# Optimization experiments

Measured on AMD Instinct MI355X. Metric: run time of the kernel, lower is better.

The kernel has to match this reference:

```python
import jax, jax.numpy as jnp
import numpy as np

N, K, F_IN, F_OUT = 32768, 16, 128, 128
NEG_SLOPE = 0.2  # LeakyReLU slope in original module


def setup_inputs() -> dict:
    key = jax.random.key(0)
    ks = jax.random.split(key, 8)
    nodes = jax.random.normal(ks[0], (N, F_IN), dtype=jnp.float32)
    neighbors = jax.random.normal(ks[1], (N, K, F_IN), dtype=jnp.float32)
    aspects = jax.random.normal(ks[2], (N, K, F_IN), dtype=jnp.float32)
    attention_scores = jax.random.uniform(ks[3], (N, K), dtype=jnp.float32)
    # Parameters (torch.nn.Linear stores weight as [out, in])
    lim_w = float(np.sqrt(6.0 / (F_IN + F_OUT)))  # xavier_uniform
    W = jax.random.uniform(ks[4], (F_OUT, F_IN), minval=-lim_w, maxval=lim_w, dtype=jnp.float32)
    lim_a = float(np.sqrt(6.0 / (2 * F_IN + F_OUT)))
    Wa = jax.random.uniform(ks[5], (F_OUT, 2 * F_IN), minval=-lim_a, maxval=lim_a, dtype=jnp.float32)
    ba = jax.random.uniform(ks[6], (F_OUT,), minval=-0.05, maxval=0.05, dtype=jnp.float32)
    bias = jnp.zeros((F_OUT,), dtype=jnp.float32)
    return {"nodes": nodes, "neighbors": neighbors, "aspects": aspects,
            "attention_scores": attention_scores, "W": W, "Wa": Wa, "ba": ba, "bias": bias}


def reference(nodes, neighbors, aspects, attention_scores, W, Wa, ba, bias):
    # linear_proj (no bias); dropout(p=0.01) treated as eval/identity
    node_proj = nodes @ W.T                                  # [N, F_OUT]
    neigh_proj = jnp.einsum('nkf,of->nko', neighbors, W)     # [N, K, F_OUT]
    asp_proj = jnp.einsum('nkf,of->nko', aspects, W)         # [N, K, F_OUT]
    # aspects_method == 'linear': cat(neigh_proj, asp_proj) then Linear(2F->F)
    cat = jnp.concatenate([neigh_proj, asp_proj], axis=-1)   # [N, K, 2*F_OUT]
    nap = jnp.einsum('nkf,of->nko', cat, Wa) + ba            # [N, K, F_OUT]
    # per-edge: leakyReLU(nap + broadcast target node proj).exp()
    features_per_edge = jnp.exp(jax.nn.leaky_relu(nap + node_proj[:, None, :], NEG_SLOPE))
    # weight by attention score and sum over neighbors (scatter-sum per node)
    out = jnp.sum(features_per_edge * attention_scores[..., None], axis=1)  # [N, F_OUT]
    # skip_concat_bias: concat=True -> view [N, F_OUT], add bias, ELU activation
    return jax.nn.elu(out + bias)
```

## Files before the change

kernel.cpp:

```cpp
#include <hip/hip_runtime.h>
#include <hip/hip_bf16.h>
#include <stdint.h>

typedef short bf16x8 __attribute__((ext_vector_type(8)));
typedef float f32x4  __attribute__((ext_vector_type(4)));

#define NNODES    32768
#define KNB       16
#define FDIM      128
#define NEG_SLOPE 0.2f
#define NBLK      512
#define PPB       (NNODES / (2 * NBLK))

static __device__ __forceinline__ unsigned short f2bf(float x) {
  union { float f; unsigned u; } v; v.f = x;
  unsigned r = v.u + 0x7fffu + ((v.u >> 16) & 1u);
  return (unsigned short)(r >> 16);
}

static __device__ __forceinline__ bf16x8 pack8(f32x4 lo, f32x4 hi) {
  union { __hip_bfloat162 h[4]; bf16x8 v; } u;
  u.h[0] = __float22bfloat162_rn(make_float2(lo[0], lo[1]));
  u.h[1] = __float22bfloat162_rn(make_float2(lo[2], lo[3]));
  u.h[2] = __float22bfloat162_rn(make_float2(hi[0], hi[1]));
  u.h[3] = __float22bfloat162_rn(make_float2(hi[2], hi[3]));
  return u.v;
}

static __device__ __forceinline__ void storeBL(unsigned short* BL, int ct, int l16,
                                               int col, unsigned short v) {
  const int kc = col >> 5, quad = (col >> 3) & 3, j = col & 7;
  BL[(size_t)(((kc * 8 + ct) * 64) + quad * 16 + l16) * 8 + j] = v;
}

__global__ void prep_weights(const float* __restrict__ W,
                             const float* __restrict__ Wa,
                             unsigned short* __restrict__ BL) {
  const int o = blockIdx.x;
  const int f = threadIdx.x;
  const float* war = Wa + o * 256;
  float a1 = 0.f, a2 = 0.f;
  #pragma unroll 8
  for (int j = 0; j < 128; ++j) {
    float w = W[j * 128 + f];
    a1 = fmaf(war[j], w, a1);
    a2 = fmaf(war[128 + j], w, a2);
  }
  const int ct = o >> 4, l16 = o & 15;
  storeBL(BL, ct, l16, f,       f2bf(a1));
  storeBL(BL, ct, l16, 128 + f, f2bf(a2));
  storeBL(BL, ct, l16, 256 + f, f2bf(W[o * 128 + f]));
}

__global__ __launch_bounds__(512, 4)
void grn_main(const float* __restrict__ nodes,
              const float* __restrict__ neighbors,
              const float* __restrict__ aspects,
              const float* __restrict__ scores,
              const unsigned short* __restrict__ BL,
              const float* __restrict__ ba,
              const float* __restrict__ bias,
              float* __restrict__ out) {
  const int tid  = threadIdx.x;
  const int lane = tid & 63;
  const int w    = tid >> 6;
  const int quad = lane >> 4;
  const int l16  = lane & 15;

  __shared__ __align__(16) unsigned short Aeg[2][8192];
  __shared__ __align__(16) unsigned short And[2][256];
  __shared__ float xp[2][2][FDIM];

  bf16x8 breg[12];
  #pragma unroll
  for (int kc = 0; kc < 12; ++kc)
    breg[kc] = *(const bf16x8*)(BL + ((size_t)(kc * 8 + w) * 64 + lane) * 8);

  const float ba_c = ba[w * 16 + l16];
  float bias_t = 0.f;
  if (tid < 256) bias_t = bias[tid & 127];

  const int seg = tid >> 8;
  const int row = (tid >> 4) & 15;
  const int c16 = tid & 15;
  const int cc  = seg * 16 + c16;
  const float* segp = seg ? aspects : neighbors;
  const int wroff = row * 512 + ((cc * 16) ^ ((row & 7) << 4));
  const int sw    = (l16 & 7) << 4;
  const int rdrow = l16 * 512;

  const int pair0 = blockIdx.x * PPB;

  f32x4 eg[2][2];
  f32x4 nd[2];

  {
    const size_t ng = (size_t)pair0 * 2;
    #pragma unroll
    for (int n = 0; n < 2; ++n) {
      const float* src = segp + ((ng + n) * KNB + row) * FDIM + c16 * 8;
      eg[n][0] = *(const f32x4*)src;
      eg[n][1] = *(const f32x4*)(src + 4);
    }
    if (tid < 32) {
      const float* nsrc = nodes + (ng + (tid >> 4)) * FDIM + (tid & 15) * 8;
      nd[0] = *(const f32x4*)nsrc;
      nd[1] = *(const f32x4*)(nsrc + 4);
    }
    #pragma unroll
    for (int n = 0; n < 2; ++n)
      *(bf16x8*)((char*)Aeg[0] + n * 8192 + wroff) = pack8(eg[n][0], eg[n][1]);
    if (tid < 32)
      *(bf16x8*)((char*)And[0] + tid * 16) = pack8(nd[0], nd[1]);
  }
  __syncthreads();

  for (int i = 0; i < PPB; ++i) {
    const int buf = i & 1;
    const size_t ng = (size_t)(pair0 + i) * 2;

    if (i + 1 < PPB) {
      const size_t ng2 = ng + 2;
      #pragma unroll
      for (int n = 0; n < 2; ++n) {
        const float* src = segp + ((ng2 + n) * KNB + row) * FDIM + c16 * 8;
        eg[n][0] = *(const f32x4*)src;
        eg[n][1] = *(const f32x4*)(src + 4);
      }
      if (tid < 32) {
        const float* nsrc = nodes + (ng2 + (tid >> 4)) * FDIM + (tid & 15) * 8;
        nd[0] = *(const f32x4*)nsrc;
        nd[1] = *(const f32x4*)(nsrc + 4);
      }
    }

    f32x4 acc[2];
    acc[0] = (f32x4){0.f, 0.f, 0.f, 0.f};
    acc[1] = (f32x4){0.f, 0.f, 0.f, 0.f};
    const char* ab = (const char*)Aeg[buf];
    const char* nb = (const char*)And[buf];
    #pragma unroll
    for (int n = 0; n < 2; ++n) {
      #pragma unroll
      for (int kc = 0; kc < 8; ++kc) {
        bf16x8 af = *(const bf16x8*)(ab + n * 8192 + rdrow +
                                     (((kc * 4 + quad) * 16) ^ sw));
        acc[n] = __builtin_amdgcn_mfma_f32_16x16x32_bf16(af, breg[kc], acc[n], 0, 0, 0);
      }
      #pragma unroll
      for (int kn = 0; kn < 4; ++kn) {
        bf16x8 af = *(const bf16x8*)(nb + (n * 16 + kn * 4 + quad) * 16);
        acc[n] = __builtin_amdgcn_mfma_f32_16x16x32_bf16(af, breg[8 + kn], acc[n], 0, 0, 0);
      }
    }

    #pragma unroll
    for (int n = 0; n < 2; ++n) {
      f32x4 sc = *(const f32x4*)(scores + (ng + n) * KNB + quad * 4);
      float s = 0.f;
      #pragma unroll
      for (int r = 0; r < 4; ++r) {
        float t  = acc[n][r] + ba_c;
        float lr = t > 0.f ? t : NEG_SLOPE * t;
        s = fmaf(__expf(lr), sc[r], s);
      }
      s += __shfl_xor(s, 16);
      s += __shfl_xor(s, 32);
      if (quad == 0) xp[buf][n][w * 16 + l16] = s;
    }

    if (i + 1 < PPB) {
      const int nbuf = buf ^ 1;
      #pragma unroll
      for (int n = 0; n < 2; ++n)
        *(bf16x8*)((char*)Aeg[nbuf] + n * 8192 + wroff) = pack8(eg[n][0], eg[n][1]);
      if (tid < 32)
        *(bf16x8*)((char*)And[nbuf] + tid * 16) = pack8(nd[0], nd[1]);
    }
    __syncthreads();

    if (tid < 256) {
      const int n = tid >> 7, c = tid & 127;
      float v = xp[buf][n][c] + bias_t;
      v = v > 0.f ? v : __expf(v) - 1.f;
      out[(ng + n) * FDIM + c] = v;
    }
  }
}

extern "C" void kernel_launch(void* const* d_in, const int* in_sizes, int n_in,
                              void* d_out, int out_size, void* d_ws, size_t ws_size,
                              hipStream_t stream) {
  const float* nodes     = (const float*)d_in[0];
  const float* neighbors = (const float*)d_in[1];
  const float* aspects   = (const float*)d_in[2];
  const float* scores    = (const float*)d_in[3];
  const float* W         = (const float*)d_in[4];
  const float* Wa        = (const float*)d_in[5];
  const float* ba        = (const float*)d_in[6];
  const float* bias      = (const float*)d_in[7];
  unsigned short* BL     = (unsigned short*)d_ws;

  prep_weights<<<128, 128, 0, stream>>>(W, Wa, BL);
  grn_main<<<NBLK, 512, 0, stream>>>(nodes, neighbors, aspects, scores,
                                     BL, ba, bias, (float*)d_out);
}
```

Measured before the change: 547.1 us.

## Process four nodes per iteration with fragment-major LDS layout and staged scores

```diff
diff --git a/kernel.cpp b/kernel.cpp
--- a/kernel.cpp
+++ b/kernel.cpp
@@ -10,7 +10,7 @@
 #define FDIM      128
 #define NEG_SLOPE 0.2f
 #define NBLK      512
-#define PPB       (NNODES / (2 * NBLK))
+#define ITERS     (NNODES / (4 * NBLK))
 
 static __device__ __forceinline__ unsigned short f2bf(float x) {
   union { float f; unsigned u; } v; v.f = x;
@@ -67,123 +67,119 @@
   const int quad = lane >> 4;
   const int l16  = lane & 15;
 
-  __shared__ __align__(16) unsigned short Aeg[2][8192];
-  __shared__ __align__(16) unsigned short And[2][256];
-  __shared__ float xp[2][2][FDIM];
+  __shared__ __align__(16) unsigned short Afr[2][4][8][512];
+  __shared__ __align__(16) unsigned short Andl[2][4][128];
+  __shared__ float xp[2][4][FDIM];
+  __shared__ float scl[2][4][KNB];
 
   bf16x8 breg[12];
   #pragma unroll
   for (int kc = 0; kc < 12; ++kc)
     breg[kc] = *(const bf16x8*)(BL + ((size_t)(kc * 8 + w) * 64 + lane) * 8);
 
-  const float ba_c = ba[w * 16 + l16];
-  float bias_t = 0.f;
-  if (tid < 256) bias_t = bias[tid & 127];
+  const float ba_c   = ba[w * 16 + l16];
+  const float bias_t = bias[tid & 127];
 
   const int seg = tid >> 8;
   const int row = (tid >> 4) & 15;
   const int c16 = tid & 15;
-  const int cc  = seg * 16 + c16;
   const float* segp = seg ? aspects : neighbors;
-  const int wroff = row * 512 + ((cc * 16) ^ ((row & 7) << 4));
-  const int sw    = (l16 & 7) << 4;
-  const int rdrow = l16 * 512;
-
-  const int pair0 = blockIdx.x * PPB;
-
-  f32x4 eg[2][2];
-  f32x4 nd[2];
-
-  {
-    const size_t ng = (size_t)pair0 * 2;
-    #pragma unroll
-    for (int n = 0; n < 2; ++n) {
-      const float* src = segp + ((ng + n) * KNB + row) * FDIM + c16 * 8;
-      eg[n][0] = *(const f32x4*)src;
-      eg[n][1] = *(const f32x4*)(src + 4);
-    }
-    if (tid < 32) {
-      const float* nsrc = nodes + (ng + (tid >> 4)) * FDIM + (tid & 15) * 8;
-      nd[0] = *(const f32x4*)nsrc;
-      nd[1] = *(const f32x4*)(nsrc + 4);
-    }
-    #pragma unroll
-    for (int n = 0; n < 2; ++n)
-      *(bf16x8*)((char*)Aeg[0] + n * 8192 + wroff) = pack8(eg[n][0], eg[n][1]);
-    if (tid < 32)
-      *(bf16x8*)((char*)And[0] + tid * 16) = pack8(nd[0], nd[1]);
-  }
+  const int kcw   = seg * 4 + (c16 >> 2);
+  const int qw    = c16 & 3;
+  const int slotw = ((qw * 16) | (row ^ (qw << 1))) ^ kcw;
+  const int wroff = kcw * 1024 + slotw * 16;
+  const int sl16  = ((quad * 16) | (l16 ^ (quad << 1))) * 16;
+
+  const int node0 = blockIdx.x * (ITERS * 4);
+
+  f32x4 eg[4][2];
+  f32x4 nd2[2];
+  f32x4 scv;
+
+  auto issue_loads = [&](int j) {
+    const size_t nb0 = (size_t)node0 + (size_t)j * 4;
+    #pragma unroll
+    for (int m = 0; m < 4; ++m) {
+      const float* src = segp + ((nb0 + m) * KNB + row) * FDIM + c16 * 8;
+      eg[m][0] = *(const f32x4*)src;
+      eg[m][1] = *(const f32x4*)(src + 4);
+    }
+    if (tid < 64) {
+      const float* nsrc = nodes + (nb0 + (tid >> 4)) * FDIM + (tid & 15) * 8;
+      nd2[0] = *(const f32x4*)nsrc;
+      nd2[1] = *(const f32x4*)(nsrc + 4);
+    }
+    if (tid < 16)
+      scv = *(const f32x4*)(scores + (nb0 + (tid >> 2)) * KNB + (tid & 3) * 4);
+  };
+
+  auto write_stage = [&](int b) {
+    char* abase = (char*)Afr + b * 32768;
+    #pragma unroll
+    for (int m = 0; m < 4; ++m)
+      *(bf16x8*)(abase + m * 8192 + wroff) = pack8(eg[m][0], eg[m][1]);
+    if (tid < 64)
+      *(bf16x8*)((char*)Andl + b * 1024 + tid * 16) = pack8(nd2[0], nd2[1]);
+    if (tid < 16)
+      *(f32x4*)&scl[b][tid >> 2][(tid & 3) * 4] = scv;
+  };
+
+  issue_loads(0);
+  write_stage(0);
   __syncthreads();
 
-  for (int i = 0; i < PPB; ++i) {
+  for (int i = 0; i < ITERS; ++i) {
     const int buf = i & 1;
-    const size_t ng = (size_t)(pair0 + i) * 2;
-
-    if (i + 1 < PPB) {
-      const size_t ng2 = ng + 2;
+    if (i + 1 < ITERS) issue_loads(i + 1);
+
+    f32x4 acc[4];
+    #pragma unroll
+    for (int m = 0; m < 4; ++m) acc[m] = (f32x4){0.f, 0.f, 0.f, 0.f};
+
+    const char* ab = (const char*)Afr + buf * 32768;
+    const char* nb = (const char*)Andl + buf * 1024;
+    #pragma unroll
+    for (int kc = 0; kc < 8; ++kc) {
+      const int off = kc * 1024 + (sl16 ^ (kc << 4));
       #pragma unroll
-      for (int n = 0; n < 2; ++n) {
-        const float* src = segp + ((ng2 + n) * KNB + row) * FDIM + c16 * 8;
-        eg[n][0] = *(const f32x4*)src;
-        eg[n][1] = *(const f32x4*)(src + 4);
+      for (int m = 0; m < 4; ++m) {
+        bf16x8 af = *(const bf16x8*)(ab + m * 8192 + off);
+        acc[m] = __builtin_amdgcn_mfma_f32_16x16x32_bf16(af, breg[kc], acc[m], 0, 0, 0);
       }
-      if (tid < 32) {
-        const float* nsrc = nodes + (ng2 + (tid >> 4)) * FDIM + (tid & 15) * 8;
-        nd[0] = *(const f32x4*)nsrc;
-        nd[1] = *(const f32x4*)(nsrc + 4);
+    }
+    #pragma unroll
+    for (int kn = 0; kn < 4; ++kn) {
+      const int off = (kn * 4 + quad) * 16;
+      #pragma unroll
+      for (int m = 0; m < 4; ++m) {
+        bf16x8 af = *(const bf16x8*)(nb + m * 256 + off);
+        acc[m] = __builtin_amdgcn_mfma_f32_16x16x32_bf16(af, breg[8 + kn], acc[m], 0, 0, 0);
       }
     }
 
-    f32x4 acc[2];
-    acc[0] = (f32x4){0.f, 0.f, 0.f, 0.f};
-    acc[1] = (f32x4){0.f, 0.f, 0.f, 0.f};
-    const char* ab = (const char*)Aeg[buf];
-    const char* nb = (const char*)And[buf];
-    #pragma unroll
-    for (int n = 0; n < 2; ++n) {
-      #pragma unroll
-      for (int kc = 0; kc < 8; ++kc) {
-        bf16x8 af = *(const bf16x8*)(ab + n * 8192 + rdrow +
-                                     (((kc * 4 + quad) * 16) ^ sw));
-        acc[n] = __builtin_amdgcn_mfma_f32_16x16x32_bf16(af, breg[kc], acc[n], 0, 0, 0);
-      }
-      #pragma unroll
-      for (int kn = 0; kn < 4; ++kn) {
-        bf16x8 af = *(const bf16x8*)(nb + (n * 16 + kn * 4 + quad) * 16);
-        acc[n] = __builtin_amdgcn_mfma_f32_16x16x32_bf16(af, breg[8 + kn], acc[n], 0, 0, 0);
-      }
-    }
-
-    #pragma unroll
-    for (int n = 0; n < 2; ++n) {
-      f32x4 sc = *(const f32x4*)(scores + (ng + n) * KNB + quad * 4);
+    #pragma unroll
+    for (int m = 0; m < 4; ++m) {
+      f32x4 sc = *(const f32x4*)&scl[buf][m][quad * 4];
       float s = 0.f;
       #pragma unroll
       for (int r = 0; r < 4; ++r) {
-        float t  = acc[n][r] + ba_c;
+        float t  = acc[m][r] + ba_c;
         float lr = t > 0.f ? t : NEG_SLOPE * t;
         s = fmaf(__expf(lr), sc[r], s);
       }
       s += __shfl_xor(s, 16);
       s += __shfl_xor(s, 32);
-      if (quad == 0) xp[buf][n][w * 16 + l16] = s;
-    }
-
-    if (i + 1 < PPB) {
-      const int nbuf = buf ^ 1;
-      #pragma unroll
-      for (int n = 0; n < 2; ++n)
-        *(bf16x8*)((char*)Aeg[nbuf] + n * 8192 + wroff) = pack8(eg[n][0], eg[n][1]);
-      if (tid < 32)
-        *(bf16x8*)((char*)And[nbuf] + tid * 16) = pack8(nd[0], nd[1]);
-    }
+      if (quad == 0) xp[buf][m][w * 16 + l16] = s;
+    }
+
+    if (i + 1 < ITERS) write_stage(buf ^ 1);
     __syncthreads();
 
-    if (tid < 256) {
+    {
       const int n = tid >> 7, c = tid & 127;
       float v = xp[buf][n][c] + bias_t;
       v = v > 0.f ? v : __expf(v) - 1.f;
-      out[(ng + n) * FDIM + c] = v;
+      out[((size_t)node0 + i * 4 + n) * FDIM + c] = v;
     }
   }
 }
```

After: 564.5 us. 1.03x slower.
